# Performance work log

Hardware: AMD Instinct MI355X
Metric: run time of the kernel (lower is better)

The kernel has to match this reference:

```python
import jax, jax.numpy as jnp
import numpy as np

L, B, T, C, H = 8, 2, 1024, 1024, 16
DH = C // H          # 64, head dim (even, required for RoPE)
DFF = 4 * C          # 4096
THETA = 10000.0
EPS = 1e-5


def _ln(x, scale, bias):
    m = jnp.mean(x, axis=-1, keepdims=True)
    v = jnp.mean((x - m) ** 2, axis=-1, keepdims=True)
    return (x - m) * jax.lax.rsqrt(v + EPS) * scale + bias


def _rope_cos_sin():
    # matches precompute_freqs_cis: freqs_cis[t, j] = exp(i * t * theta^{-2j/dim})
    inv = 1.0 / (THETA ** (jnp.arange(0, DH, 2, dtype=jnp.float32) / DH))  # (DH/2,)
    ang = jnp.arange(T, dtype=jnp.float32)[:, None] * inv[None, :]         # (T, DH/2)
    return jnp.cos(ang), jnp.sin(ang)


def _apply_rope(x, cos, sin):
    # x: (B,H,T,DH); complex multiply on interleaved pairs == torch.view_as_complex path
    xr = x.reshape(B, H, T, DH // 2, 2)
    x0, x1 = xr[..., 0], xr[..., 1]
    o0 = x0 * cos - x1 * sin
    o1 = x0 * sin + x1 * cos
    return jnp.stack([o0, o1], axis=-1).reshape(B, H, T, DH)


def setup_inputs() -> dict:
    key = jax.random.key(0)
    ks = jax.random.split(key, 20)
    s = 0.02
    p = lambda k, shape: (jax.random.normal(k, shape, jnp.float32) * s)
    return {
        "x": jax.random.normal(ks[0], (B, T, C), jnp.float32),
        "Wq": p(ks[1], (L, C, C)), "bq": jnp.zeros((L, C), jnp.float32),
        "Wk": p(ks[2], (L, C, C)), "bk": jnp.zeros((L, C), jnp.float32),
        "Wv": p(ks[3], (L, C, C)), "bv": jnp.zeros((L, C), jnp.float32),
        "Wo": p(ks[4], (L, C, C)), "bo": jnp.zeros((L, C), jnp.float32),
        "ln1_s": jnp.ones((L, C), jnp.float32), "ln1_b": jnp.zeros((L, C), jnp.float32),
        "ln2_s": jnp.ones((L, C), jnp.float32), "ln2_b": jnp.zeros((L, C), jnp.float32),
        "W1": p(ks[5], (L, C, DFF)), "b1": jnp.zeros((L, DFF), jnp.float32),
        "W2": p(ks[6], (L, DFF, C)), "b2": jnp.zeros((L, C), jnp.float32),
        "lnf_s": jnp.ones((C,), jnp.float32), "lnf_b": jnp.zeros((C,), jnp.float32),
    }


def reference(x, Wq, bq, Wk, bk, Wv, bv, Wo, bo,
              ln1_s, ln1_b, ln2_s, ln2_b, W1, b1, W2, b2, lnf_s, lnf_b):
    cos, sin = _rope_cos_sin()
    causal = jnp.tril(jnp.ones((T, T), bool))
    inv_sqrt_dh = jnp.float32(1.0 / np.sqrt(DH))

    def layer(h, p):
        wq, bq_, wk, bk_, wv, bv_, wo, bo_, s1, c1, s2, c2, w1, d1, w2, d2 = p
        a = _ln(h, s1, c1)
        q = (a @ wq + bq_).reshape(B, T, H, DH).transpose(0, 2, 1, 3)  # (B,H,T,DH)
        k = (a @ wk + bk_).reshape(B, T, H, DH).transpose(0, 2, 1, 3)
        v = (a @ wv + bv_).reshape(B, T, H, DH).transpose(0, 2, 1, 3)
        q = _apply_rope(q, cos, sin)
        k = _apply_rope(k, cos, sin)
        att = jnp.einsum('bhqd,bhkd->bhqk', q, k) * inv_sqrt_dh
        att = jnp.where(causal, att, -jnp.inf)
        att = jax.nn.softmax(att, axis=-1)
        y = jnp.einsum('bhqk,bhkd->bhqd', att, v)
        y = y.transpose(0, 2, 1, 3).reshape(B, T, C)
        h = h + (y @ wo + bo_)
        m = _ln(h, s2, c2)
        h = h + (jax.nn.gelu(m @ w1 + d1, approximate=False) @ w2 + d2)
        return h, None

    h, _ = jax.lax.scan(
        layer, x,
        (Wq, bq, Wk, bk, Wv, bv, Wo, bo, ln1_s, ln1_b, ln2_s, ln2_b, W1, b1, W2, b2))
    return _ln(h, lnf_s, lnf_b)
```

## Files before the change

### kernel.cpp

```cpp
#include <hip/hip_runtime.h>
#include <cstdint>
#include <cstddef>

#define L_   8
#define B_   2
#define T_   1024
#define C_   1024
#define H_   16
#define DH_  64
#define DFF_ 4096
#define M_   2048

typedef __attribute__((ext_vector_type(4))) float f32x4;
typedef __attribute__((ext_vector_type(8))) short short8_t;
typedef __attribute__((ext_vector_type(8))) __bf16 bf16x8_t;
typedef __attribute__((ext_vector_type(4))) unsigned short ushort4_t;
typedef __attribute__((ext_vector_type(8))) unsigned short ushort8_t;

__device__ __forceinline__ float bf2f(unsigned short u) {
  unsigned int i = ((unsigned int)u) << 16;
  return __builtin_bit_cast(float, i);
}
__device__ __forceinline__ unsigned short f2bf(float f) {
  unsigned int u = __builtin_bit_cast(unsigned int, f);
  u += 0x7fff + ((u >> 16) & 1);
  return (unsigned short)(u >> 16);
}
__device__ __forceinline__ f32x4 mfma16x16x32(short8_t a, short8_t b, f32x4 c) {
  return __builtin_amdgcn_mfma_f32_16x16x32_bf16(
      __builtin_bit_cast(bf16x8_t, a), __builtin_bit_cast(bf16x8_t, b), c, 0, 0, 0);
}
__device__ __forceinline__ void async_copy16(const void* g, void* l) {
  __builtin_amdgcn_global_load_lds(
      (const __attribute__((address_space(1))) unsigned int*)g,
      (__attribute__((address_space(3))) unsigned int*)l, 16, 0, 0);
}

__global__ __launch_bounds__(256) void convert_k(
    const float* __restrict__ Wq, const float* __restrict__ Wk,
    const float* __restrict__ Wv, const float* __restrict__ Wo,
    const float* __restrict__ W1, const float* __restrict__ W2,
    unsigned short* __restrict__ wt) {
  __shared__ float tile[64][68];
  const int bx = blockIdx.x;
  const int layer = bx / 3072;
  const int r = bx - layer * 3072;
  const float* src; unsigned short* dst; int R, Cc, t;
  unsigned short* wl = wt + (size_t)layer * 12582912;
  if (r < 768) {
    const int mat = r >> 8; t = r & 255;
    src = (mat == 0 ? Wq : mat == 1 ? Wk : Wv) + (size_t)layer * 1048576;
    dst = wl + (size_t)mat * 1048576; R = 1024; Cc = 1024;
  } else if (r < 1024) {
    t = r - 768; src = Wo + (size_t)layer * 1048576;
    dst = wl + 3145728; R = 1024; Cc = 1024;
  } else if (r < 2048) {
    t = r - 1024; src = W1 + (size_t)layer * 4194304;
    dst = wl + 4194304; R = 1024; Cc = 4096;
  } else {
    t = r - 2048; src = W2 + (size_t)layer * 4194304;
    dst = wl + 8388608; R = 4096; Cc = 1024;
  }
  const int nTc = Cc >> 6;
  const int tr = t / nTc, tc = t - tr * nTc;
  const int r0 = tr * 64, c0 = tc * 64;
  const int tid = threadIdx.x;
  const int tx = tid & 15, ty = tid >> 4;
#pragma unroll
  for (int i = 0; i < 4; ++i) {
    const int row = ty + 16 * i;
    const float4 v = *(const float4*)(src + (size_t)(r0 + row) * Cc + c0 + tx * 4);
    *(float4*)&tile[row][tx * 4] = v;
  }
  __syncthreads();
#pragma unroll
  for (int pass = 0; pass < 2; ++pass) {
    const int chunk = pass * 256 + tid;
    const int c = chunk >> 3;
    const int off = (chunk & 7) * 8;
    ushort8_t val;
#pragma unroll
    for (int j = 0; j < 8; ++j) val[j] = f2bf(tile[off + j][c]);
    *(ushort8_t*)(dst + (size_t)(c0 + c) * R + r0 + off) = val;
  }
}

__global__ __launch_bounds__(256) void ln_k(const float* __restrict__ X,
                                            const float* __restrict__ gam,
                                            const float* __restrict__ bet,
                                            unsigned short* __restrict__ out) {
  const int row = blockIdx.x;
  const int tid = threadIdx.x;
  const int lane = tid & 63, w = tid >> 6;
  const float4 v = ((const float4*)(X + (size_t)row * C_))[tid];
  float sum = v.x + v.y + v.z + v.w;
  float sq  = v.x*v.x + v.y*v.y + v.z*v.z + v.w*v.w;
#pragma unroll
  for (int d = 1; d < 64; d <<= 1) {
    sum += __shfl_xor(sum, d, 64);
    sq  += __shfl_xor(sq,  d, 64);
  }
  __shared__ float red[8];
  if (lane == 0) { red[w] = sum; red[4 + w] = sq; }
  __syncthreads();
  sum = red[0] + red[1] + red[2] + red[3];
  sq  = red[4] + red[5] + red[6] + red[7];
  const float mean = sum * (1.0f / C_);
  const float var  = sq * (1.0f / C_) - mean * mean;
  const float inv  = rsqrtf(var + 1e-5f);
  const int col = tid * 4;
  const float xs[4] = { v.x, v.y, v.z, v.w };
  ushort4_t ov;
#pragma unroll
  for (int i = 0; i < 4; ++i)
    ov[i] = f2bf((xs[i]-mean)*inv*gam[col+i] + bet[col+i]);
  *(ushort4_t*)(out + (size_t)row * C_ + col) = ov;
}

template<int NS, int FINAL>
__global__ __launch_bounds__(256) void reduce_ln(
    float* __restrict__ h, const float* __restrict__ bias,
    const float* __restrict__ part,
    const float* __restrict__ gam, const float* __restrict__ bet,
    void* __restrict__ out) {
  const int row = blockIdx.x;
  const int tid = threadIdx.x;
  const int lane = tid & 63, w = tid >> 6;
  const size_t base = (size_t)row * C_;
  float4 v = ((const float4*)(h + base))[tid];
  const float4 b = ((const float4*)bias)[tid];
  v.x += b.x; v.y += b.y; v.z += b.z; v.w += b.w;
#pragma unroll
  for (int z = 0; z < NS; ++z) {
    const float4 p = ((const float4*)(part + (size_t)z * M_ * C_ + base))[tid];
    v.x += p.x; v.y += p.y; v.z += p.z; v.w += p.w;
  }
  if (!FINAL) ((float4*)(h + base))[tid] = v;
  float sum = v.x + v.y + v.z + v.w;
  float sq  = v.x*v.x + v.y*v.y + v.z*v.z + v.w*v.w;
#pragma unroll
  for (int d = 1; d < 64; d <<= 1) {
    sum += __shfl_xor(sum, d, 64);
    sq  += __shfl_xor(sq,  d, 64);
  }
  __shared__ float red[8];
  if (lane == 0) { red[w] = sum; red[4 + w] = sq; }
  __syncthreads();
  sum = red[0] + red[1] + red[2] + red[3];
  sq  = red[4] + red[5] + red[6] + red[7];
  const float mean = sum * (1.0f / C_);
  const float var  = sq * (1.0f / C_) - mean * mean;
  const float inv  = rsqrtf(var + 1e-5f);
  const float4 g  = ((const float4*)gam)[tid];
  const float4 be = ((const float4*)bet)[tid];
  if (FINAL) {
    float4 ov;
    ov.x = (v.x-mean)*inv*g.x + be.x;
    ov.y = (v.y-mean)*inv*g.y + be.y;
    ov.z = (v.z-mean)*inv*g.z + be.z;
    ov.w = (v.w-mean)*inv*g.w + be.w;
    ((float4*)out)[(size_t)row * 256 + tid] = ov;
  } else {
    ushort4_t ov;
    const float xs[4] = { v.x, v.y, v.z, v.w };
    const float gs[4] = { g.x, g.y, g.z, g.w };
    const float bs[4] = { be.x, be.y, be.z, be.w };
#pragma unroll
    for (int i = 0; i < 4; ++i)
      ov[i] = f2bf((xs[i]-mean)*inv*gs[i] + bs[i]);
    *(ushort4_t*)((unsigned short*)out + base + tid * 4) = ov;
  }
}

template<int EPI>
__global__ __launch_bounds__(256) void gemm64(
    const unsigned short* __restrict__ A,
    const unsigned short* __restrict__ Bt,
    const float* __restrict__ bias0,
    const float* __restrict__ bias1,
    const float* __restrict__ bias2,
    void* __restrict__ out0, void* __restrict__ out1, void* __restrict__ out2,
    int M, int N, int K) {
  __shared__ __align__(16) unsigned short As[64 * 32];
  __shared__ __align__(16) unsigned short Bs[128 * 32];
  const int tid = threadIdx.x;
  const int lane = tid & 63;
  const int w = tid >> 6;
  const int ln15 = lane & 15, lg = lane >> 4;
  const int row0 = blockIdx.y * 64, col0 = blockIdx.x * 128;
  const int wr = w >> 1, wc = w & 1;

  const int kper = K / gridDim.z;
  const int k0 = blockIdx.z * kper;

  f32x4 acc[2][4] = {};

  const int rA  = tid >> 2,          ccA = (tid & 3) * 8;
  const int rB0 = tid >> 2,          ccB = (tid & 3) * 8;
  const int rB1 = (256 + tid) >> 2;

  for (int kt = k0; kt < k0 + kper; kt += 32) {
    async_copy16(A  + (size_t)(row0 + rA)  * K + kt + ccA, (char*)As + ((size_t)w * 64) * 16);
    async_copy16(Bt + (size_t)(col0 + rB0) * K + kt + ccB, (char*)Bs + ((size_t)w * 64) * 16);
    async_copy16(Bt + (size_t)(col0 + rB1) * K + kt + ccB, (char*)Bs + ((size_t)(256 + w * 64)) * 16);
    __syncthreads();
    short8_t af[2], bfr[4];
#pragma unroll
    for (int m = 0; m < 2; ++m)
      af[m] = *(const short8_t*)(As + (wr*32 + m*16 + ln15) * 32 + lg * 8);
#pragma unroll
    for (int n = 0; n < 4; ++n)
      bfr[n] = *(const short8_t*)(Bs + (wc*64 + n*16 + ln15) * 32 + lg * 8);
#pragma unroll
    for (int m = 0; m < 2; ++m)
#pragma unroll
      for (int n = 0; n < 4; ++n)
        acc[m][n] = mfma16x16x32(af[m], bfr[n], acc[m][n]);
    __syncthreads();
  }

#pragma unroll
  for (int m = 0; m < 2; ++m) {
#pragma unroll
    for (int n = 0; n < 4; ++n) {
#pragma unroll
      for (int r = 0; r < 4; ++r) {
        const int rg = row0 + wr*32 + m*16 + lg*4 + r;
        const int cg = col0 + wc*64 + n*16 + ln15;
        float v = acc[m][n][r];
        if (EPI == 0) {
          if (cg < 2048) {
            v += (cg < 1024) ? bias0[cg] : bias1[cg - 1024];
            const float vp = __shfl_xor(v, 1, 64);
            const int j = (cg & 63) >> 1;
            const float ang = (float)(rg & 1023) *
                              exp2f((float)j * -0.41524101186092029f);
            float sn, cs;
            sincosf(ang, &sn, &cs);
            const float ov = (cg & 1) ? (vp * sn + v * cs) : (v * cs - vp * sn);
            unsigned short* dstp = (cg < 1024) ? (unsigned short*)out0
                                               : (unsigned short*)out1;
            dstp[(size_t)rg * C_ + (cg & 1023)] = f2bf(ov);
          } else {
            const int ch = cg - 2048;
            v += bias2[ch];
            const int hh = ch >> 6, dh = ch & 63;
            const int bb = rg >> 10, t = rg & 1023;
            ((unsigned short*)out2)[(((size_t)(bb * H_ + hh) * DH_ + dh) << 10) + t] = f2bf(v);
          }
        } else {
          ((float*)out0)[((size_t)blockIdx.z * M_ + rg) * (size_t)N + cg] = v;
        }
      }
    }
  }
}

__global__ __launch_bounds__(256) void gemm128_gelu(
    const unsigned short* __restrict__ A,
    const unsigned short* __restrict__ Bt,
    const float* __restrict__ bias,
    unsigned short* __restrict__ out,
    int M, int N, int K) {
  __shared__ __align__(16) unsigned short As[128 * 32];
  __shared__ __align__(16) unsigned short Bs[128 * 32];
  const int tid = threadIdx.x;
  const int lane = tid & 63;
  const int w = tid >> 6;
  const int ln15 = lane & 15, lg = lane >> 4;
  const int row0 = blockIdx.y * 128, col0 = blockIdx.x * 128;
  const int wr = w >> 1, wc = w & 1;

  f32x4 acc[4][4] = {};

  const int r0s = tid >> 2,         cc0 = (tid & 3) * 8;
  const int r1s = (256 + tid) >> 2, cc1 = (tid & 3) * 8;

  for (int kt = 0; kt < K; kt += 32) {
    async_copy16(A  + (size_t)(row0 + r0s) * K + kt + cc0, (char*)As + ((size_t)w * 64) * 16);
    async_copy16(A  + (size_t)(row0 + r1s) * K + kt + cc1, (char*)As + ((size_t)(256 + w * 64)) * 16);
    async_copy16(Bt + (size_t)(col0 + r0s) * K + kt + cc0, (char*)Bs + ((size_t)w * 64) * 16);
    async_copy16(Bt + (size_t)(col0 + r1s) * K + kt + cc1, (char*)Bs + ((size_t)(256 + w * 64)) * 16);
    __syncthreads();
    short8_t af[4], bfr[4];
#pragma unroll
    for (int m = 0; m < 4; ++m)
      af[m] = *(const short8_t*)(As + (wr*64 + m*16 + ln15) * 32 + lg * 8);
#pragma unroll
    for (int n = 0; n < 4; ++n)
      bfr[n] = *(const short8_t*)(Bs + (wc*64 + n*16 + ln15) * 32 + lg * 8);
#pragma unroll
    for (int m = 0; m < 4; ++m)
#pragma unroll
      for (int n = 0; n < 4; ++n)
        acc[m][n] = mfma16x16x32(af[m], bfr[n], acc[m][n]);
    __syncthreads();
  }

#pragma unroll
  for (int m = 0; m < 4; ++m) {
#pragma unroll
    for (int n = 0; n < 4; ++n) {
#pragma unroll
      for (int r = 0; r < 4; ++r) {
        const int rg = row0 + wr*64 + m*16 + lg*4 + r;
        const int cg = col0 + wc*64 + n*16 + ln15;
        float v = acc[m][n][r] + bias[cg];
        v = 0.5f * v * (1.0f + erff(v * 0.70710678118654752f));
        out[(size_t)rg * N + cg] = f2bf(v);
      }
    }
  }
}

#define PSTR 136

template<bool MASK>
__device__ __forceinline__ void attn_tile(
    const int kb, const int ln15, const int lg, const int rowg0,
    const unsigned short* __restrict__ Kp,
    const unsigned short* __restrict__ Vp,
    const short8_t aq0, const short8_t aq1,
    float* __restrict__ m_run, float* __restrict__ l_run,
    f32x4* __restrict__ o, unsigned short* __restrict__ P) {
  const unsigned short* kt = Kp + (size_t)kb * 128 * C_;
  const unsigned short* vt = Vp + kb * 128;
  f32x4 s[8];
#pragma unroll
  for (int n = 0; n < 8; ++n) {
    const short8_t b0 = *(const short8_t*)(kt + (size_t)n * 16 * C_);
    const short8_t b1 = *(const short8_t*)(kt + (size_t)n * 16 * C_ + 32);
    f32x4 z = {};
    z = mfma16x16x32(aq0, b0, z);
    s[n] = mfma16x16x32(aq1, b1, z);
  }
  short8_t vb[4][4];
#pragma unroll
  for (int c = 0; c < 4; ++c)
#pragma unroll
    for (int n = 0; n < 4; ++n)
      vb[c][n] = *(const short8_t*)(vt + (size_t)n * 16 * T_ + c * 32);

  const float SCL = 0.18033688011116012f;
  float mx[4];
#pragma unroll
  for (int r = 0; r < 4; ++r) {
    float mr = -1e30f;
#pragma unroll
    for (int n = 0; n < 8; ++n) {
      float v = s[n][r] * SCL;
      if (MASK && (kb * 128 + n * 16 + ln15) > (rowg0 + r)) v = -1e30f;
      s[n][r] = v;
      mr = fmaxf(mr, v);
    }
    mx[r] = mr;
  }
#pragma unroll
  for (int d = 1; d < 16; d <<= 1)
#pragma unroll
    for (int r = 0; r < 4; ++r) mx[r] = fmaxf(mx[r], __shfl_xor(mx[r], d, 64));
#pragma unroll
  for (int r = 0; r < 4; ++r) {
    const float mn = fmaxf(m_run[r], mx[r]);
    const float scf = exp2f(m_run[r] - mn);
    m_run[r] = mn;
    float rs = 0.0f;
#pragma unroll
    for (int n = 0; n < 8; ++n) {
      const float pv = exp2f(s[n][r] - mn);
      s[n][r] = pv;
      rs += pv;
    }
#pragma unroll
    for (int d = 1; d < 16; d <<= 1) rs += __shfl_xor(rs, d, 64);
    l_run[r] = l_run[r] * scf + rs;
#pragma unroll
    for (int n = 0; n < 4; ++n) o[n][r] *= scf;
  }
  __syncthreads();
#pragma unroll
  for (int r = 0; r < 4; ++r)
#pragma unroll
    for (int n = 0; n < 8; ++n)
      P[(lg * 4 + r) * PSTR + n * 16 + ln15] = f2bf(s[n][r]);
  __syncthreads();
#pragma unroll
  for (int c = 0; c < 4; ++c) {
    const short8_t pa = *(const short8_t*)(P + ln15 * PSTR + c * 32 + lg * 8);
#pragma unroll
    for (int n = 0; n < 4; ++n)
      o[n] = mfma16x16x32(pa, vb[c][n], o[n]);
  }
}

__global__ __launch_bounds__(64) void attn_k(const unsigned short* __restrict__ Q,
                                             const unsigned short* __restrict__ Kb,
                                             const unsigned short* __restrict__ Vt,
                                             unsigned short* __restrict__ Y) {
  __shared__ __align__(16) unsigned short P[16 * PSTR];
  const int lane = threadIdx.x;
  const int ln15 = lane & 15, lg = lane >> 4;
  const int qt = blockIdx.x, bh = blockIdx.y;
  const int b = bh >> 4, h = bh & 15;
  const int q0 = qt * 16;

  short8_t aq0, aq1;
  {
    const unsigned short* qp = Q + ((size_t)(b * T_ + q0 + ln15)) * C_ + h * DH_ + lg * 8;
    aq0 = *(const short8_t*)(qp);
    aq1 = *(const short8_t*)(qp + 32);
  }
  float m_run[4] = { -1e30f, -1e30f, -1e30f, -1e30f };
  float l_run[4] = {};
  f32x4 o[4] = {};
  const int rowg0 = q0 + lg * 4;
  const unsigned short* Kp = Kb + ((size_t)b * T_ + ln15) * C_ + h * DH_ + lg * 8;
  const unsigned short* Vp = Vt + ((size_t)bh * DH_ + ln15) * T_ + lg * 8;

  const int kb_last = qt >> 3;
  for (int kb = 0; kb < kb_last; ++kb)
    attn_tile<false>(kb, ln15, lg, rowg0, Kp, Vp, aq0, aq1, m_run, l_run, o, P);
  attn_tile<true>(kb_last, ln15, lg, rowg0, Kp, Vp, aq0, aq1, m_run, l_run, o, P);

#pragma unroll
  for (int n = 0; n < 4; ++n)
#pragma unroll
    for (int r = 0; r < 4; ++r) {
      const float val = o[n][r] / l_run[r];
      Y[((size_t)(b * T_ + rowg0 + r)) * C_ + h * DH_ + n * 16 + ln15] = f2bf(val);
    }
}

extern "C" void kernel_launch(void* const* d_in, const int* in_sizes, int n_in,
                              void* d_out, int out_size, void* d_ws, size_t ws_size,
                              hipStream_t stream) {
  const float* x    = (const float*)d_in[0];
  const float* Wq   = (const float*)d_in[1];
  const float* bq   = (const float*)d_in[2];
  const float* Wk   = (const float*)d_in[3];
  const float* bk   = (const float*)d_in[4];
  const float* Wv   = (const float*)d_in[5];
  const float* bv   = (const float*)d_in[6];
  const float* Wo   = (const float*)d_in[7];
  const float* bo   = (const float*)d_in[8];
  const float* ln1s = (const float*)d_in[9];
  const float* ln1b = (const float*)d_in[10];
  const float* ln2s = (const float*)d_in[11];
  const float* ln2b = (const float*)d_in[12];
  const float* W1   = (const float*)d_in[13];
  const float* b1   = (const float*)d_in[14];
  const float* W2   = (const float*)d_in[15];
  const float* b2   = (const float*)d_in[16];
  const float* lnfs = (const float*)d_in[17];
  const float* lnfb = (const float*)d_in[18];

  const size_t MB = (size_t)1 << 20;
  char* ws = (char*)d_ws;
  float*          h      = (float*)(ws + 0);
  unsigned short* a_bf   = (unsigned short*)(ws + 8*MB);
  unsigned short* q_bf   = (unsigned short*)(ws + 12*MB);
  unsigned short* k_bf   = (unsigned short*)(ws + 16*MB);
  unsigned short* vt_bf  = (unsigned short*)(ws + 20*MB);
  unsigned short* y_bf   = (unsigned short*)(ws + 24*MB);
  unsigned short* mid_bf = (unsigned short*)(ws + 28*MB);
  float*          part   = (float*)(ws + 44*MB);
  unsigned short* wt_all = (unsigned short*)(ws + 76*MB);

  convert_k<<<8 * 3072, 256, 0, stream>>>(Wq, Wk, Wv, Wo, W1, W2, wt_all);
  hipMemcpyAsync(h, x, (size_t)M_ * C_ * sizeof(float), hipMemcpyDeviceToDevice, stream);
  ln_k<<<M_, 256, 0, stream>>>(h, ln1s, ln1b, a_bf);

  for (int l = 0; l < L_; ++l) {
    const unsigned short* wt_l = wt_all + (size_t)l * 12582912;
    gemm64<0><<<dim3(24, 32, 1), 256, 0, stream>>>(a_bf, wt_l,
        bq + l*C_, bk + l*C_, bv + l*C_, q_bf, k_bf, vt_bf, M_, 3*C_, C_);
    attn_k<<<dim3(T_/16, B_*H_), 64, 0, stream>>>(q_bf, k_bf, vt_bf, y_bf);
    gemm64<3><<<dim3(8, 32, 2), 256, 0, stream>>>(y_bf, wt_l + 3145728,
        nullptr, nullptr, nullptr, part, nullptr, nullptr, M_, C_, C_);
    reduce_ln<2, 0><<<M_, 256, 0, stream>>>(h, bo + l*C_, part,
        ln2s + l*C_, ln2b + l*C_, a_bf);
    gemm128_gelu<<<dim3(32, 16), 256, 0, stream>>>(a_bf, wt_l + 4194304,
        b1 + l*DFF_, mid_bf, M_, DFF_, C_);
    gemm64<3><<<dim3(8, 32, 4), 256, 0, stream>>>(mid_bf, wt_l + 8388608,
        nullptr, nullptr, nullptr, part, nullptr, nullptr, M_, C_, DFF_);
    if (l < L_ - 1) {
      reduce_ln<4, 0><<<M_, 256, 0, stream>>>(h, b2 + l*C_, part,
          ln1s + (l+1)*C_, ln1b + (l+1)*C_, a_bf);
    } else {
      reduce_ln<4, 1><<<M_, 256, 0, stream>>>(h, b2 + l*C_, part,
          lnfs, lnfb, d_out);
    }
  }
}
```

Baseline: 1.853 ms.

## Split causal attention across key chunks with a separate combine kernel

```diff
diff --git a/kernel.cpp b/kernel.cpp
--- a/kernel.cpp
+++ b/kernel.cpp
@@ -41,7 +41,7 @@
     const float* __restrict__ Wv, const float* __restrict__ Wo,
     const float* __restrict__ W1, const float* __restrict__ W2,
     unsigned short* __restrict__ wt) {
-  __shared__ float tile[64][68];
+  __shared__ float tile[64 * 64];
   const int bx = blockIdx.x;
   const int layer = bx / 3072;
   const int r = bx - layer * 3072;
@@ -70,18 +70,21 @@
   for (int i = 0; i < 4; ++i) {
     const int row = ty + 16 * i;
     const float4 v = *(const float4*)(src + (size_t)(r0 + row) * Cc + c0 + tx * 4);
-    *(float4*)&tile[row][tx * 4] = v;
+    const int uw = (tx + (row >> 3)) & 15;
+    *(float4*)&tile[row * 64 + uw * 4] = v;
   }
   __syncthreads();
 #pragma unroll
   for (int pass = 0; pass < 2; ++pass) {
     const int chunk = pass * 256 + tid;
     const int c = chunk >> 3;
-    const int off = (chunk & 7) * 8;
+    const int og = chunk & 7;
+    const int ur = ((c >> 2) + og) & 15;
+    const int col = ur * 4 + (c & 3);
     ushort8_t val;
 #pragma unroll
-    for (int j = 0; j < 8; ++j) val[j] = f2bf(tile[off + j][c]);
-    *(ushort8_t*)(dst + (size_t)(c0 + c) * R + r0 + off) = val;
+    for (int j = 0; j < 8; ++j) val[j] = f2bf(tile[(og * 8 + j) * 64 + col]);
+    *(ushort8_t*)(dst + (size_t)(c0 + c) * R + r0 + og * 8) = val;
   }
 }
 
@@ -317,14 +320,14 @@
 
 template<bool MASK>
 __device__ __forceinline__ void attn_tile(
-    const int kb, const int ln15, const int lg, const int rowg0,
+    const int g, const int ln15, const int lg, const int rowg0,
     const unsigned short* __restrict__ Kp,
     const unsigned short* __restrict__ Vp,
     const short8_t aq0, const short8_t aq1,
     float* __restrict__ m_run, float* __restrict__ l_run,
     f32x4* __restrict__ o, unsigned short* __restrict__ P) {
-  const unsigned short* kt = Kp + (size_t)kb * 128 * C_;
-  const unsigned short* vt = Vp + kb * 128;
+  const unsigned short* kt = Kp + (size_t)g * 128 * C_;
+  const unsigned short* vt = Vp + g * 128;
   f32x4 s[8];
 #pragma unroll
   for (int n = 0; n < 8; ++n) {
@@ -349,7 +352,7 @@
 #pragma unroll
     for (int n = 0; n < 8; ++n) {
       float v = s[n][r] * SCL;
-      if (MASK && (kb * 128 + n * 16 + ln15) > (rowg0 + r)) v = -1e30f;
+      if (MASK && (g * 128 + n * 16 + ln15) > (rowg0 + r)) v = -1e30f;
       s[n][r] = v;
       mr = fmaxf(mr, v);
     }
@@ -396,11 +399,15 @@
 __global__ __launch_bounds__(64) void attn_k(const unsigned short* __restrict__ Q,
                                              const unsigned short* __restrict__ Kb,
                                              const unsigned short* __restrict__ Vt,
-                                             unsigned short* __restrict__ Y) {
+                                             float* __restrict__ o_part,
+                                             float2* __restrict__ ml_part) {
+  const int qt = blockIdx.x, bh = blockIdx.y, hh = blockIdx.z;
+  const int dt = qt >> 3;
+  const int diag_h = dt >> 1;
+  if (hh > diag_h) return;
   __shared__ __align__(16) unsigned short P[16 * PSTR];
   const int lane = threadIdx.x;
   const int ln15 = lane & 15, lg = lane >> 4;
-  const int qt = blockIdx.x, bh = blockIdx.y;
   const int b = bh >> 4, h = bh & 15;
   const int q0 = qt * 16;
 
@@ -417,18 +424,49 @@
   const unsigned short* Kp = Kb + ((size_t)b * T_ + ln15) * C_ + h * DH_ + lg * 8;
   const unsigned short* Vp = Vt + ((size_t)bh * DH_ + ln15) * T_ + lg * 8;
 
-  const int kb_last = qt >> 3;
-  for (int kb = 0; kb < kb_last; ++kb)
-    attn_tile<false>(kb, ln15, lg, rowg0, Kp, Vp, aq0, aq1, m_run, l_run, o, P);
-  attn_tile<true>(kb_last, ln15, lg, rowg0, Kp, Vp, aq0, aq1, m_run, l_run, o, P);
-
-#pragma unroll
-  for (int n = 0; n < 4; ++n)
-#pragma unroll
-    for (int r = 0; r < 4; ++r) {
-      const float val = o[n][r] / l_run[r];
-      Y[((size_t)(b * T_ + rowg0 + r)) * C_ + h * DH_ + n * 16 + ln15] = f2bf(val);
-    }
+  if (hh < diag_h) {
+    attn_tile<false>(hh * 2,     ln15, lg, rowg0, Kp, Vp, aq0, aq1, m_run, l_run, o, P);
+    attn_tile<false>(hh * 2 + 1, ln15, lg, rowg0, Kp, Vp, aq0, aq1, m_run, l_run, o, P);
+  } else {
+    if (dt & 1)
+      attn_tile<false>(hh * 2, ln15, lg, rowg0, Kp, Vp, aq0, aq1, m_run, l_run, o, P);
+    attn_tile<true>(dt, ln15, lg, rowg0, Kp, Vp, aq0, aq1, m_run, l_run, o, P);
+  }
+
+  const size_t obase = ((((size_t)hh * 32 + bh) << 10) + rowg0) * 64;
+#pragma unroll
+  for (int r = 0; r < 4; ++r) {
+#pragma unroll
+    for (int n = 0; n < 4; ++n)
+      o_part[obase + (size_t)r * 64 + n * 16 + ln15] = o[n][r];
+    if (ln15 == 0)
+      ml_part[(((size_t)hh * 32 + bh) << 10) + rowg0 + r] =
+          make_float2(m_run[r], l_run[r]);
+  }
+}
+
+__global__ __launch_bounds__(256) void attn_combine(
+    const float* __restrict__ o_part, const float2* __restrict__ ml_part,
+    unsigned short* __restrict__ Y) {
+  const int tid = threadIdx.x;
+  const int row_id = blockIdx.x * 4 + (tid >> 6);
+  const int lane = tid & 63;
+  const int bh = row_id >> 10, t = row_id & 1023;
+  const int nact = (t >> 8) + 1;
+  float m = -1e30f;
+  float2 ml[4];
+  for (int hh = 0; hh < nact; ++hh) {
+    ml[hh] = ml_part[(((size_t)hh * 32 + bh) << 10) + t];
+    m = fmaxf(m, ml[hh].x);
+  }
+  float L = 0.0f, O = 0.0f;
+  for (int hh = 0; hh < nact; ++hh) {
+    const float wgt = exp2f(ml[hh].x - m);
+    L += ml[hh].y * wgt;
+    O += o_part[((((size_t)hh * 32 + bh) << 10) + t) * 64 + lane] * wgt;
+  }
+  const int b = bh >> 4, h = bh & 15;
+  Y[((size_t)(b * T_ + t)) * C_ + h * DH_ + lane] = f2bf(O / L);
 }
 
 extern "C" void kernel_launch(void* const* d_in, const int* in_sizes, int n_in,
@@ -465,6 +503,8 @@
   unsigned short* mid_bf = (unsigned short*)(ws + 28*MB);
   float*          part   = (float*)(ws + 44*MB);
   unsigned short* wt_all = (unsigned short*)(ws + 76*MB);
+  float*          o_part = (float*)(ws + 268*MB);
+  float2*         ml_prt = (float2*)(ws + 300*MB);
 
   convert_k<<<8 * 3072, 256, 0, stream>>>(Wq, Wk, Wv, Wo, W1, W2, wt_all);
   hipMemcpyAsync(h, x, (size_t)M_ * C_ * sizeof(float), hipMemcpyDeviceToDevice, stream);
@@ -474,7 +514,9 @@
     const unsigned short* wt_l = wt_all + (size_t)l * 12582912;
     gemm64<0><<<dim3(24, 32, 1), 256, 0, stream>>>(a_bf, wt_l,
         bq + l*C_, bk + l*C_, bv + l*C_, q_bf, k_bf, vt_bf, M_, 3*C_, C_);
-    attn_k<<<dim3(T_/16, B_*H_), 64, 0, stream>>>(q_bf, k_bf, vt_bf, y_bf);
+    attn_k<<<dim3(T_/16, B_*H_, 4), 64, 0, stream>>>(q_bf, k_bf, vt_bf,
+        o_part, ml_prt);
+    attn_combine<<<(B_*H_*T_)/4, 256, 0, stream>>>(o_part, ml_prt, y_bf);
     gemm64<3><<<dim3(8, 32, 2), 256, 0, stream>>>(y_bf, wt_l + 3145728,
         nullptr, nullptr, nullptr, part, nullptr, nullptr, M_, C_, C_);
     reduce_ln<2, 0><<<M_, 256, 0, stream>>>(h, bo + l*C_, part,
```

New measurement: 1.986 ms. 7.2% more time.

## Use 128-tile split-K GEMM for FFN down-projection and swizzle convert tile

Applied to the files above, without the earlier changes.

```diff
diff --git a/kernel.cpp b/kernel.cpp
--- a/kernel.cpp
+++ b/kernel.cpp
@@ -41,7 +41,7 @@
     const float* __restrict__ Wv, const float* __restrict__ Wo,
     const float* __restrict__ W1, const float* __restrict__ W2,
     unsigned short* __restrict__ wt) {
-  __shared__ float tile[64][68];
+  __shared__ float tile[64 * 64];
   const int bx = blockIdx.x;
   const int layer = bx / 3072;
   const int r = bx - layer * 3072;
@@ -70,18 +70,21 @@
   for (int i = 0; i < 4; ++i) {
     const int row = ty + 16 * i;
     const float4 v = *(const float4*)(src + (size_t)(r0 + row) * Cc + c0 + tx * 4);
-    *(float4*)&tile[row][tx * 4] = v;
+    const int uw = (tx + (row >> 3)) & 15;
+    *(float4*)&tile[row * 64 + uw * 4] = v;
   }
   __syncthreads();
 #pragma unroll
   for (int pass = 0; pass < 2; ++pass) {
     const int chunk = pass * 256 + tid;
     const int c = chunk >> 3;
-    const int off = (chunk & 7) * 8;
+    const int og = chunk & 7;
+    const int ur = ((c >> 2) + og) & 15;
+    const int col = ur * 4 + (c & 3);
     ushort8_t val;
 #pragma unroll
-    for (int j = 0; j < 8; ++j) val[j] = f2bf(tile[off + j][c]);
-    *(ushort8_t*)(dst + (size_t)(c0 + c) * R + r0 + off) = val;
+    for (int j = 0; j < 8; ++j) val[j] = f2bf(tile[(og * 8 + j) * 64 + col]);
+    *(ushort8_t*)(dst + (size_t)(c0 + c) * R + r0 + og * 8) = val;
   }
 }
 
@@ -256,11 +259,12 @@
   }
 }
 
-__global__ __launch_bounds__(256) void gemm128_gelu(
+template<int EPI>
+__global__ __launch_bounds__(256) void gemm128(
     const unsigned short* __restrict__ A,
     const unsigned short* __restrict__ Bt,
     const float* __restrict__ bias,
-    unsigned short* __restrict__ out,
+    void* __restrict__ out,
     int M, int N, int K) {
   __shared__ __align__(16) unsigned short As[128 * 32];
   __shared__ __align__(16) unsigned short Bs[128 * 32];
@@ -271,12 +275,15 @@
   const int row0 = blockIdx.y * 128, col0 = blockIdx.x * 128;
   const int wr = w >> 1, wc = w & 1;
 
+  const int kper = K / gridDim.z;
+  const int k0 = blockIdx.z * kper;
+
   f32x4 acc[4][4] = {};
 
   const int r0s = tid >> 2,         cc0 = (tid & 3) * 8;
   const int r1s = (256 + tid) >> 2, cc1 = (tid & 3) * 8;
 
-  for (int kt = 0; kt < K; kt += 32) {
+  for (int kt = k0; kt < k0 + kper; kt += 32) {
     async_copy16(A  + (size_t)(row0 + r0s) * K + kt + cc0, (char*)As + ((size_t)w * 64) * 16);
     async_copy16(A  + (size_t)(row0 + r1s) * K + kt + cc1, (char*)As + ((size_t)(256 + w * 64)) * 16);
     async_copy16(Bt + (size_t)(col0 + r0s) * K + kt + cc0, (char*)Bs + ((size_t)w * 64) * 16);
@@ -305,9 +312,14 @@
       for (int r = 0; r < 4; ++r) {
         const int rg = row0 + wr*64 + m*16 + lg*4 + r;
         const int cg = col0 + wc*64 + n*16 + ln15;
-        float v = acc[m][n][r] + bias[cg];
-        v = 0.5f * v * (1.0f + erff(v * 0.70710678118654752f));
-        out[(size_t)rg * N + cg] = f2bf(v);
+        float v = acc[m][n][r];
+        if (EPI == 2) {
+          v += bias[cg];
+          v = 0.5f * v * (1.0f + erff(v * 0.70710678118654752f));
+          ((unsigned short*)out)[(size_t)rg * N + cg] = f2bf(v);
+        } else {
+          ((float*)out)[((size_t)blockIdx.z * M_ + rg) * (size_t)N + cg] = v;
+        }
       }
     }
   }
@@ -317,14 +329,14 @@
 
 template<bool MASK>
 __device__ __forceinline__ void attn_tile(
-    const int kb, const int ln15, const int lg, const int rowg0,
+    const int g, const int ln15, const int lg, const int rowg0,
     const unsigned short* __restrict__ Kp,
     const unsigned short* __restrict__ Vp,
     const short8_t aq0, const short8_t aq1,
     float* __restrict__ m_run, float* __restrict__ l_run,
     f32x4* __restrict__ o, unsigned short* __restrict__ P) {
-  const unsigned short* kt = Kp + (size_t)kb * 128 * C_;
-  const unsigned short* vt = Vp + kb * 128;
+  const unsigned short* kt = Kp + (size_t)g * 128 * C_;
+  const unsigned short* vt = Vp + g * 128;
   f32x4 s[8];
 #pragma unroll
   for (int n = 0; n < 8; ++n) {
@@ -349,7 +361,7 @@
 #pragma unroll
     for (int n = 0; n < 8; ++n) {
       float v = s[n][r] * SCL;
-      if (MASK && (kb * 128 + n * 16 + ln15) > (rowg0 + r)) v = -1e30f;
+      if (MASK && (g * 128 + n * 16 + ln15) > (rowg0 + r)) v = -1e30f;
       s[n][r] = v;
       mr = fmaxf(mr, v);
     }
@@ -479,10 +491,10 @@
         nullptr, nullptr, nullptr, part, nullptr, nullptr, M_, C_, C_);
     reduce_ln<2, 0><<<M_, 256, 0, stream>>>(h, bo + l*C_, part,
         ln2s + l*C_, ln2b + l*C_, a_bf);
-    gemm128_gelu<<<dim3(32, 16), 256, 0, stream>>>(a_bf, wt_l + 4194304,
+    gemm128<2><<<dim3(32, 16, 1), 256, 0, stream>>>(a_bf, wt_l + 4194304,
         b1 + l*DFF_, mid_bf, M_, DFF_, C_);
-    gemm64<3><<<dim3(8, 32, 4), 256, 0, stream>>>(mid_bf, wt_l + 8388608,
-        nullptr, nullptr, nullptr, part, nullptr, nullptr, M_, C_, DFF_);
+    gemm128<3><<<dim3(8, 16, 4), 256, 0, stream>>>(mid_bf, wt_l + 8388608,
+        nullptr, part, M_, C_, DFF_);
     if (l < L_ - 1) {
       reduce_ln<4, 0><<<M_, 256, 0, stream>>>(h, b2 + l*C_, part,
           ln1s + (l+1)*C_, ln1b + (l+1)*C_, a_bf);
```

Result: no change. 1.818 ms (-1.9%).
